# Performance work log

Hardware: AMD Instinct MI355X
Metric: run time of the kernel (lower is better)

## Reference

```python
import jax, jax.numpy as jnp
import numpy as np

PYRAMID_BINS = [512, 256, 128, 64]
ENTRY_CHANNELS = 14
CONV_FILTERS = 4
HIDDEN = 64
BATCH = 2048
LENGTH = 2048
NEG_SLOPE = 0.01  # LeakyReLU default


def setup_inputs() -> dict:
    key = jax.random.key(0)
    ks = jax.random.split(key, 9)
    nb = len(PYRAMID_BINS)
    return {
        "X": jax.random.normal(ks[0], (BATCH, ENTRY_CHANNELS, LENGTH), jnp.float32),
        "conv_w": jax.random.normal(ks[1], (nb, CONV_FILTERS, ENTRY_CHANNELS, 3), jnp.float32) * 0.1,
        "conv_b": jax.random.normal(ks[2], (nb, CONV_FILTERS), jnp.float32) * 0.1,
        "w_ih": jax.random.normal(ks[3], (nb, 4 * HIDDEN, CONV_FILTERS), jnp.float32) * 0.1,
        "w_hh": jax.random.normal(ks[4], (nb, 4 * HIDDEN, HIDDEN), jnp.float32) * 0.1,
        "b_ih": jax.random.normal(ks[5], (nb, 4 * HIDDEN), jnp.float32) * 0.1,
        "b_hh": jax.random.normal(ks[6], (nb, 4 * HIDDEN), jnp.float32) * 0.1,
        "lin_w": jax.random.normal(ks[7], (nb, 1, HIDDEN), jnp.float32) * 0.1,
        "lin_b": jax.random.normal(ks[8], (nb, 1), jnp.float32) * 0.1,
    }


def adaptive_avg_pool1d(x, out_size):
    # matches torch F.avg_pool1d with stride = L//out, kernel = L-(out-1)*stride
    L = x.shape[-1]
    stride = L // out_size
    kernel = L - (out_size - 1) * stride
    idx = jnp.arange(out_size)[:, None] * stride + jnp.arange(kernel)[None, :]  # (out, k)
    return x[..., idx].mean(axis=-1)  # (B, C, out)


def conv1d_same(x, w, b):
    # x: (B,C,L), w: (O,I,3), padding=1 -> same length
    y = jax.lax.conv_general_dilated(x, w, window_strides=(1,), padding=((1, 1),),
                                     dimension_numbers=("NCH", "OIH", "NCH"))
    return y + b[None, :, None]


def lstm_scan(xs, w_ih, w_hh, b_ih, b_hh):
    # xs: (T, B, in); PyTorch LSTMCell gate order (i, f, g, o)
    B = xs.shape[1]
    h0 = jnp.zeros((B, HIDDEN), xs.dtype)
    c0 = jnp.zeros((B, HIDDEN), xs.dtype)

    def step(carry, x):
        h, c = carry
        gates = x @ w_ih.T + b_ih + h @ w_hh.T + b_hh  # (B, 4H)
        i, f, g, o = jnp.split(gates, 4, axis=-1)
        i = jax.nn.sigmoid(i)
        f = jax.nn.sigmoid(f)
        g = jnp.tanh(g)
        o = jax.nn.sigmoid(o)
        c = f * c + i * g
        h = o * jnp.tanh(c)
        return (h, c), None

    (h, _), _ = jax.lax.scan(step, (h0, c0), xs)
    return h  # final hidden (B, H)


def reference(X, conv_w, conv_b, w_ih, w_hh, b_ih, b_hh, lin_w, lin_b):
    outs = []
    for i, bin_size in enumerate(PYRAMID_BINS):
        xp = adaptive_avg_pool1d(X, bin_size)                  # (B, C, bin)
        xc = conv1d_same(xp, conv_w[i], conv_b[i])             # (B, 4, bin)
        xc = jnp.where(xc >= 0, xc, NEG_SLOPE * xc)            # LeakyReLU
        xs = jnp.transpose(xc, (2, 0, 1))                      # (T, B, 4)
        h = lstm_scan(xs, w_ih[i], w_hh[i], b_ih[i], b_hh[i])  # (B, H)
        outs.append(h @ lin_w[i].T + lin_b[i])                 # (B, 1)
    return jnp.concatenate(outs, axis=1)                       # (B, n_bins)
```

## Files before the change

### kernel.cpp

```cpp
#include <hip/hip_runtime.h>
#include <math.h>

#define BATCH 2048
#define CIN 14
#define LEN 2048
#define NB 4
#define HID 64
#define NEG 0.01f
#define L2E 1.44269504088896f

typedef __attribute__((ext_vector_type(8))) _Float16 f16x8;
typedef __attribute__((ext_vector_type(4))) float f32x4;

__device__ __forceinline__ void conv_bin(const float* __restrict__ P, int ldp, int T,
                                         int bin,
                                         const float* __restrict__ cw,
                                         const float* __restrict__ cb,
                                         float* __restrict__ dst, int tid)
{
    const float* w = cw + (size_t)bin * 4 * CIN * 3;
    const float b0 = cb[bin * 4 + 0];
    const float b1 = cb[bin * 4 + 1];
    const float b2 = cb[bin * 4 + 2];
    const float b3 = cb[bin * 4 + 3];
    for (int t = tid; t < T; t += 256) {
        float a0 = b0, a1 = b1, a2 = b2, a3 = b3;
        for (int ci = 0; ci < CIN; ++ci) {
            float pm = (t > 0)     ? P[ci * ldp + t - 1] : 0.0f;
            float p0 =               P[ci * ldp + t];
            float pp = (t < T - 1) ? P[ci * ldp + t + 1] : 0.0f;
            const float* w0 = w + (0 * CIN + ci) * 3;
            const float* w1 = w + (1 * CIN + ci) * 3;
            const float* w2 = w + (2 * CIN + ci) * 3;
            const float* w3 = w + (3 * CIN + ci) * 3;
            a0 += w0[0] * pm + w0[1] * p0 + w0[2] * pp;
            a1 += w1[0] * pm + w1[1] * p0 + w1[2] * pp;
            a2 += w2[0] * pm + w2[1] * p0 + w2[2] * pp;
            a3 += w3[0] * pm + w3[1] * p0 + w3[2] * pp;
        }
        a0 = (a0 >= 0.0f) ? a0 : NEG * a0;
        a1 = (a1 >= 0.0f) ? a1 : NEG * a1;
        a2 = (a2 >= 0.0f) ? a2 : NEG * a2;
        a3 = (a3 >= 0.0f) ? a3 : NEG * a3;
        *reinterpret_cast<float4*>(dst + (size_t)t * 4) = make_float4(a0, a1, a2, a3);
    }
}

__global__ __launch_bounds__(256) void pool_conv_kernel(
    const float* __restrict__ X, const float* __restrict__ cw,
    const float* __restrict__ cb, float* __restrict__ xc)
{
    __shared__ float Pa[CIN][512];
    __shared__ float Pb[CIN][256];
    const int b = blockIdx.x;
    const int tid = threadIdx.x;

    for (int idx = tid; idx < CIN * 512; idx += 256) {
        int c = idx >> 9, t = idx & 511;
        const float4 v = *reinterpret_cast<const float4*>(X + ((size_t)b * CIN + c) * LEN + 4 * t);
        Pa[c][t] = 0.25f * (v.x + v.y + v.z + v.w);
    }
    __syncthreads();

    conv_bin(&Pa[0][0], 512, 512, 0, cw, cb, xc + (size_t)b * 512 * 4, tid);
    for (int idx = tid; idx < CIN * 256; idx += 256) {
        int c = idx >> 8, t = idx & 255;
        Pb[c][t] = 0.5f * (Pa[c][2 * t] + Pa[c][2 * t + 1]);
    }
    __syncthreads();

    conv_bin(&Pb[0][0], 256, 256, 1, cw, cb, xc + 4194304 + (size_t)b * 256 * 4, tid);
    for (int idx = tid; idx < CIN * 128; idx += 256) {
        int c = idx >> 7, t = idx & 127;
        Pa[c][t] = 0.5f * (Pb[c][2 * t] + Pb[c][2 * t + 1]);
    }
    __syncthreads();

    conv_bin(&Pa[0][0], 512, 128, 2, cw, cb, xc + 6291456 + (size_t)b * 128 * 4, tid);
    for (int idx = tid; idx < CIN * 64; idx += 256) {
        int c = idx >> 6, t = idx & 63;
        Pb[c][t] = 0.5f * (Pa[c][2 * t] + Pa[c][2 * t + 1]);
    }
    __syncthreads();

    conv_bin(&Pb[0][0], 256, 64, 3, cw, cb, xc + 7340032 + (size_t)b * 64 * 4, tid);
}


__global__ __launch_bounds__(256)
__attribute__((amdgpu_waves_per_eu(1, 1)))
void lstm_mfma_kernel(
    const float* __restrict__ xc,
    const float* __restrict__ wih, const float* __restrict__ whh,
    const float* __restrict__ bih, const float* __restrict__ bhh,
    const float* __restrict__ lw, const float* __restrict__ lb,
    float* __restrict__ out)
{
    __shared__ _Float16 hbuf[2][16][80];
    __shared__ _Float16 xbuf[16][65][8];
    __shared__ float    part[256];

    const int tid = threadIdx.x;
    const int w   = tid >> 6;
    const int l   = tid & 63;
    const int lm  = l & 15;
    const int lg  = l >> 4;

    const int TS[NB]     = {512, 256, 128, 64};
    const size_t OFF[NB] = {0, 4194304, 6291456, 7340032};

    const bool isBin0 = (blockIdx.x < 128);
    const int b0   = (isBin0 ? blockIdx.x : (blockIdx.x - 128)) * 16;
    const int binS = isBin0 ? 0 : 1;
    const int binE = isBin0 ? 1 : 4;

    for (int bin = binS; bin < binE; ++bin) {
        const int T = TS[bin];
        const int NW = T >> 6;
        const float* xbase = xc + OFF[bin];

        f16x8 whiF[4][2], xwB[4];
        f32x4 biasC[4];
        const int GMAP[4] = {2, 0, 1, 3};
        #pragma unroll
        for (int gs = 0; gs < 4; ++gs) {
            const int gate = GMAP[gs];
            const float sc = (gate == 2) ? (2.0f * L2E) : (-L2E);
            const int col = bin * 256 + gate * 64 + w * 16 + lm;
            const float* wr = whh + (size_t)col * 64;
            #pragma unroll
            for (int kt = 0; kt < 2; ++kt) {
                const float* p = wr + kt * 32 + lg * 8;
                const float4 u0 = *reinterpret_cast<const float4*>(p);
                const float4 u1 = *reinterpret_cast<const float4*>(p + 4);
                f16x8 h8;
                h8[0] = (_Float16)(sc * u0.x); h8[1] = (_Float16)(sc * u0.y);
                h8[2] = (_Float16)(sc * u0.z); h8[3] = (_Float16)(sc * u0.w);
                h8[4] = (_Float16)(sc * u1.x); h8[5] = (_Float16)(sc * u1.y);
                h8[6] = (_Float16)(sc * u1.z); h8[7] = (_Float16)(sc * u1.w);
                whiF[gs][kt] = h8;
            }
            const float4 wiv = *reinterpret_cast<const float4*>(wih + (size_t)col * 4);
            f16x8 xw;
            #pragma unroll
            for (int e = 0; e < 8; ++e) xw[e] = (_Float16)0.0f;
            if (lg == 0) {
                xw[0] = (_Float16)(sc * wiv.x); xw[1] = (_Float16)(sc * wiv.y);
                xw[2] = (_Float16)(sc * wiv.z); xw[3] = (_Float16)(sc * wiv.w);
            }
            xwB[gs] = xw;
            const float bv = (bih[col] + bhh[col]) * sc;
            biasC[gs] = (f32x4){bv, bv, bv, bv};
        }

        #pragma unroll
        for (int i = 0; i < 4; ++i) {
            const int idx = tid + i * 256;
            const int bb = idx >> 6, s = idx & 63;
            const float4 xv = *reinterpret_cast<const float4*>(
                xbase + ((size_t)(b0 + bb) * T + s) * 4);
            f16x8 pk;
            pk[0] = (_Float16)xv.x; pk[1] = (_Float16)xv.y;
            pk[2] = (_Float16)xv.z; pk[3] = (_Float16)xv.w;
            pk[4] = (_Float16)0.0f; pk[5] = (_Float16)0.0f;
            pk[6] = (_Float16)0.0f; pk[7] = (_Float16)0.0f;
            *reinterpret_cast<f16x8*>(&xbuf[bb][s][0]) = pk;
        }
        {
            _Float16* hz = &hbuf[0][0][0];
            #pragma unroll
            for (int i = 0; i < 5; ++i) hz[tid + i * 256] = (_Float16)0.0f;
        }
        float c4[4] = {0.0f, 0.0f, 0.0f, 0.0f};

        for (int tb = 0; tb < NW; ++tb) {
            float4 xr[4];
            #pragma unroll 2
            for (int tw = 0; tw < 64; ++tw) {
                if (tw == 32 && tb + 1 < NW) {
                    #pragma unroll
                    for (int i = 0; i < 4; ++i) {
                        const int idx = tid + i * 256;
                        const int bb = idx >> 6, s = idx & 63;
                        xr[i] = *reinterpret_cast<const float4*>(
                            xbase + ((size_t)(b0 + bb) * T + (tb + 1) * 64 + s) * 4);
                    }
                }
                __syncthreads();

                const int pp = tw & 1, pq = pp ^ 1;

                const f16x8 xfv = *reinterpret_cast<const f16x8*>(&xbuf[lm][tw][0]);
                const f16x8 zh0 = *reinterpret_cast<const f16x8*>(&hbuf[pp][lm][lg * 8]);
                const f16x8 zh1 = *reinterpret_cast<const f16x8*>(&hbuf[pp][lm][32 + lg * 8]);

                f32x4 aG = __builtin_amdgcn_mfma_f32_16x16x32_f16(xfv, xwB[0], biasC[0], 0, 0, 0);
                f32x4 aI = __builtin_amdgcn_mfma_f32_16x16x32_f16(xfv, xwB[1], biasC[1], 0, 0, 0);
                f32x4 aF = __builtin_amdgcn_mfma_f32_16x16x32_f16(xfv, xwB[2], biasC[2], 0, 0, 0);
                f32x4 aO = __builtin_amdgcn_mfma_f32_16x16x32_f16(xfv, xwB[3], biasC[3], 0, 0, 0);

                aG = __builtin_amdgcn_mfma_f32_16x16x32_f16(zh0, whiF[0][0], aG, 0, 0, 0);
                aG = __builtin_amdgcn_mfma_f32_16x16x32_f16(zh1, whiF[0][1], aG, 0, 0, 0);
                aI = __builtin_amdgcn_mfma_f32_16x16x32_f16(zh0, whiF[1][0], aI, 0, 0, 0);
                aI = __builtin_amdgcn_mfma_f32_16x16x32_f16(zh1, whiF[1][1], aI, 0, 0, 0);

                float eG[4];
                #pragma unroll
                for (int r = 0; r < 4; ++r)
                    eG[r] = __builtin_amdgcn_exp2f(fminf(aG[r], 120.0f));

                aF = __builtin_amdgcn_mfma_f32_16x16x32_f16(zh0, whiF[2][0], aF, 0, 0, 0);
                aF = __builtin_amdgcn_mfma_f32_16x16x32_f16(zh1, whiF[2][1], aF, 0, 0, 0);

                float rig[4];
                #pragma unroll
                for (int r = 0; r < 4; ++r) {
                    const float eI = __builtin_amdgcn_exp2f(aI[r]);
                    rig[r] = (eG[r] - 1.0f) *
                             __builtin_amdgcn_rcpf((1.0f + eI) * (eG[r] + 1.0f));
                }

                aO = __builtin_amdgcn_mfma_f32_16x16x32_f16(zh0, whiF[3][0], aO, 0, 0, 0);
                aO = __builtin_amdgcn_mfma_f32_16x16x32_f16(zh1, whiF[3][1], aO, 0, 0, 0);

                float C2[4];
                #pragma unroll
                for (int r = 0; r < 4; ++r) {
                    const float eF = __builtin_amdgcn_exp2f(aF[r]);
                    c4[r] = fmaf(__builtin_amdgcn_rcpf(1.0f + eF), c4[r], rig[r]);
                    C2[r] = __builtin_amdgcn_exp2f(
                        fminf((2.0f * L2E) * c4[r], 120.0f));
                }

                float oden[4];
                #pragma unroll
                for (int r = 0; r < 4; ++r)
                    oden[r] = 1.0f + __builtin_amdgcn_exp2f(aO[r]);

                const int u = w * 16 + lm;
                #pragma unroll
                for (int r = 0; r < 4; ++r) {
                    const float hv = (C2[r] - 1.0f) *
                        __builtin_amdgcn_rcpf(oden[r] * (C2[r] + 1.0f));
                    hbuf[pq][lg * 4 + r][u] = (_Float16)hv;
                }
            }
            if (tb + 1 < NW) {
                __syncthreads();
                #pragma unroll
                for (int i = 0; i < 4; ++i) {
                    const int idx = tid + i * 256;
                    const int bb = idx >> 6, s = idx & 63;
                    const float4 xv = xr[i];
                    f16x8 pk;
                    pk[0] = (_Float16)xv.x; pk[1] = (_Float16)xv.y;
                    pk[2] = (_Float16)xv.z; pk[3] = (_Float16)xv.w;
                    pk[4] = (_Float16)0.0f; pk[5] = (_Float16)0.0f;
                    pk[6] = (_Float16)0.0f; pk[7] = (_Float16)0.0f;
                    *reinterpret_cast<f16x8*>(&xbuf[bb][s][0]) = pk;
                }
            }
        }
        __syncthreads();

        {
            const int m = tid & 15, up = tid >> 4;
            const float* lwb = lw + bin * HID;
            float s = 0.0f;
            #pragma unroll
            for (int e = 0; e < 4; ++e) {
                const int uu = up * 4 + e;
                s = fmaf((float)hbuf[0][m][uu], lwb[uu], s);
            }
            part[tid] = s;
            __syncthreads();
            if (tid < 16) {
                float v = lb[bin];
                #pragma unroll
                for (int j = 0; j < 16; ++j) v += part[j * 16 + tid];
                out[(size_t)(b0 + tid) * NB + bin] = v;
            }
            __syncthreads();
        }
    }
}

extern "C" void kernel_launch(void* const* d_in, const int* in_sizes, int n_in,
                              void* d_out, int out_size, void* d_ws, size_t ws_size,
                              hipStream_t stream) {
    const float* X   = (const float*)d_in[0];
    const float* cw  = (const float*)d_in[1];
    const float* cb  = (const float*)d_in[2];
    const float* wih = (const float*)d_in[3];
    const float* whh = (const float*)d_in[4];
    const float* bih = (const float*)d_in[5];
    const float* bhh = (const float*)d_in[6];
    const float* lw  = (const float*)d_in[7];
    const float* lb  = (const float*)d_in[8];
    float* out = (float*)d_out;
    float* xc  = (float*)d_ws;

    pool_conv_kernel<<<BATCH, 256, 0, stream>>>(X, cw, cb, xc);
    lstm_mfma_kernel<<<256, 256, 0, stream>>>(xc, wih, whh, bih, bhh, lw, lb, out);
}
```

Before: 293.7 us.

## Process two batch tiles per LSTM block to interleave independent recurrences

Each LSTM block now handles two 16-sample batch groups with separate shared-memory h and x buffers, interleaving their MFMA and gate computations. The grid is halved to 128 blocks. The aim is to hide MFMA and transcendental latency in the serial recurrence through instruction-level parallelism, at the cost of using half as many CUs and more registers.

```diff
diff --git a/kernel.cpp b/kernel.cpp
--- a/kernel.cpp
+++ b/kernel.cpp
@@ -11,6 +11,8 @@
 
 typedef __attribute__((ext_vector_type(8))) _Float16 f16x8;
 typedef __attribute__((ext_vector_type(4))) float f32x4;
+
+#define MFMA16(A, B, C) __builtin_amdgcn_mfma_f32_16x16x32_f16((A), (B), (C), 0, 0, 0)
 
 __device__ __forceinline__ void conv_bin(const float* __restrict__ P, int ldp, int T,
                                          int bin,
@@ -96,8 +98,10 @@
     const float* __restrict__ lw, const float* __restrict__ lb,
     float* __restrict__ out)
 {
-    __shared__ _Float16 hbuf[2][16][80];
-    __shared__ _Float16 xbuf[16][65][8];
+    __shared__ _Float16 hbufA[2][16][80];
+    __shared__ _Float16 hbufB[2][16][80];
+    __shared__ _Float16 xbufA[16][65][8];
+    __shared__ _Float16 xbufB[16][65][8];
     __shared__ float    part[256];
 
     const int tid = threadIdx.x;
@@ -109,8 +113,10 @@
     const int TS[NB]     = {512, 256, 128, 64};
     const size_t OFF[NB] = {0, 4194304, 6291456, 7340032};
 
-    const bool isBin0 = (blockIdx.x < 128);
-    const int b0   = (isBin0 ? blockIdx.x : (blockIdx.x - 128)) * 16;
+    const bool isBin0 = (blockIdx.x < 64);
+    const int gid  = isBin0 ? blockIdx.x : (blockIdx.x - 64);
+    const int b0A  = gid * 32;
+    const int b0B  = b0A + 16;
     const int binS = isBin0 ? 0 : 1;
     const int binE = isBin0 ? 1 : 4;
 
@@ -157,24 +163,34 @@
         for (int i = 0; i < 4; ++i) {
             const int idx = tid + i * 256;
             const int bb = idx >> 6, s = idx & 63;
-            const float4 xv = *reinterpret_cast<const float4*>(
-                xbase + ((size_t)(b0 + bb) * T + s) * 4);
+            const float4 xvA = *reinterpret_cast<const float4*>(
+                xbase + ((size_t)(b0A + bb) * T + s) * 4);
+            const float4 xvB = *reinterpret_cast<const float4*>(
+                xbase + ((size_t)(b0B + bb) * T + s) * 4);
             f16x8 pk;
-            pk[0] = (_Float16)xv.x; pk[1] = (_Float16)xv.y;
-            pk[2] = (_Float16)xv.z; pk[3] = (_Float16)xv.w;
             pk[4] = (_Float16)0.0f; pk[5] = (_Float16)0.0f;
             pk[6] = (_Float16)0.0f; pk[7] = (_Float16)0.0f;
-            *reinterpret_cast<f16x8*>(&xbuf[bb][s][0]) = pk;
+            pk[0] = (_Float16)xvA.x; pk[1] = (_Float16)xvA.y;
+            pk[2] = (_Float16)xvA.z; pk[3] = (_Float16)xvA.w;
+            *reinterpret_cast<f16x8*>(&xbufA[bb][s][0]) = pk;
+            pk[0] = (_Float16)xvB.x; pk[1] = (_Float16)xvB.y;
+            pk[2] = (_Float16)xvB.z; pk[3] = (_Float16)xvB.w;
+            *reinterpret_cast<f16x8*>(&xbufB[bb][s][0]) = pk;
         }
         {
-            _Float16* hz = &hbuf[0][0][0];
-            #pragma unroll
-            for (int i = 0; i < 5; ++i) hz[tid + i * 256] = (_Float16)0.0f;
-        }
-        float c4[4] = {0.0f, 0.0f, 0.0f, 0.0f};
+            _Float16* hzA = &hbufA[0][0][0];
+            _Float16* hzB = &hbufB[0][0][0];
+            #pragma unroll
+            for (int i = 0; i < 5; ++i) {
+                hzA[tid + i * 256] = (_Float16)0.0f;
+                hzB[tid + i * 256] = (_Float16)0.0f;
+            }
+        }
+        float c4A[4] = {0.0f, 0.0f, 0.0f, 0.0f};
+        float c4B[4] = {0.0f, 0.0f, 0.0f, 0.0f};
 
         for (int tb = 0; tb < NW; ++tb) {
-            float4 xr[4];
+            float4 xrA[4], xrB[4];
             #pragma unroll 2
             for (int tw = 0; tw < 64; ++tw) {
                 if (tw == 32 && tb + 1 < NW) {
@@ -182,67 +198,110 @@
                     for (int i = 0; i < 4; ++i) {
                         const int idx = tid + i * 256;
                         const int bb = idx >> 6, s = idx & 63;
-                        xr[i] = *reinterpret_cast<const float4*>(
-                            xbase + ((size_t)(b0 + bb) * T + (tb + 1) * 64 + s) * 4);
+                        xrA[i] = *reinterpret_cast<const float4*>(
+                            xbase + ((size_t)(b0A + bb) * T + (tb + 1) * 64 + s) * 4);
+                        xrB[i] = *reinterpret_cast<const float4*>(
+                            xbase + ((size_t)(b0B + bb) * T + (tb + 1) * 64 + s) * 4);
                     }
                 }
                 __syncthreads();
 
                 const int pp = tw & 1, pq = pp ^ 1;
 
-                const f16x8 xfv = *reinterpret_cast<const f16x8*>(&xbuf[lm][tw][0]);
-                const f16x8 zh0 = *reinterpret_cast<const f16x8*>(&hbuf[pp][lm][lg * 8]);
-                const f16x8 zh1 = *reinterpret_cast<const f16x8*>(&hbuf[pp][lm][32 + lg * 8]);
-
-                f32x4 aG = __builtin_amdgcn_mfma_f32_16x16x32_f16(xfv, xwB[0], biasC[0], 0, 0, 0);
-                f32x4 aI = __builtin_amdgcn_mfma_f32_16x16x32_f16(xfv, xwB[1], biasC[1], 0, 0, 0);
-                f32x4 aF = __builtin_amdgcn_mfma_f32_16x16x32_f16(xfv, xwB[2], biasC[2], 0, 0, 0);
-                f32x4 aO = __builtin_amdgcn_mfma_f32_16x16x32_f16(xfv, xwB[3], biasC[3], 0, 0, 0);
-
-                aG = __builtin_amdgcn_mfma_f32_16x16x32_f16(zh0, whiF[0][0], aG, 0, 0, 0);
-                aG = __builtin_amdgcn_mfma_f32_16x16x32_f16(zh1, whiF[0][1], aG, 0, 0, 0);
-                aI = __builtin_amdgcn_mfma_f32_16x16x32_f16(zh0, whiF[1][0], aI, 0, 0, 0);
-                aI = __builtin_amdgcn_mfma_f32_16x16x32_f16(zh1, whiF[1][1], aI, 0, 0, 0);
-
-                float eG[4];
+                const f16x8 xfA  = *reinterpret_cast<const f16x8*>(&xbufA[lm][tw][0]);
+                const f16x8 zhA0 = *reinterpret_cast<const f16x8*>(&hbufA[pp][lm][lg * 8]);
+                const f16x8 zhA1 = *reinterpret_cast<const f16x8*>(&hbufA[pp][lm][32 + lg * 8]);
+                const f16x8 xfB  = *reinterpret_cast<const f16x8*>(&xbufB[lm][tw][0]);
+                const f16x8 zhB0 = *reinterpret_cast<const f16x8*>(&hbufB[pp][lm][lg * 8]);
+                const f16x8 zhB1 = *reinterpret_cast<const f16x8*>(&hbufB[pp][lm][32 + lg * 8]);
+
+                f32x4 aGA = MFMA16(xfA, xwB[0], biasC[0]);
+                f32x4 aIA = MFMA16(xfA, xwB[1], biasC[1]);
+                f32x4 aFA = MFMA16(xfA, xwB[2], biasC[2]);
+                f32x4 aOA = MFMA16(xfA, xwB[3], biasC[3]);
+                f32x4 aGB = MFMA16(xfB, xwB[0], biasC[0]);
+                f32x4 aIB = MFMA16(xfB, xwB[1], biasC[1]);
+                f32x4 aFB = MFMA16(xfB, xwB[2], biasC[2]);
+                f32x4 aOB = MFMA16(xfB, xwB[3], biasC[3]);
+
+                aGA = MFMA16(zhA0, whiF[0][0], aGA); aGA = MFMA16(zhA1, whiF[0][1], aGA);
+                aIA = MFMA16(zhA0, whiF[1][0], aIA); aIA = MFMA16(zhA1, whiF[1][1], aIA);
+                aGB = MFMA16(zhB0, whiF[0][0], aGB); aGB = MFMA16(zhB1, whiF[0][1], aGB);
+                aIB = MFMA16(zhB0, whiF[1][0], aIB); aIB = MFMA16(zhB1, whiF[1][1], aIB);
+
+                float eGA[4];
                 #pragma unroll
                 for (int r = 0; r < 4; ++r)
-                    eG[r] = __builtin_amdgcn_exp2f(fminf(aG[r], 120.0f));
-
-                aF = __builtin_amdgcn_mfma_f32_16x16x32_f16(zh0, whiF[2][0], aF, 0, 0, 0);
-                aF = __builtin_amdgcn_mfma_f32_16x16x32_f16(zh1, whiF[2][1], aF, 0, 0, 0);
-
-                float rig[4];
+                    eGA[r] = __builtin_amdgcn_exp2f(fminf(aGA[r], 120.0f));
+
+                aFA = MFMA16(zhA0, whiF[2][0], aFA); aFA = MFMA16(zhA1, whiF[2][1], aFA);
+                aFB = MFMA16(zhB0, whiF[2][0], aFB); aFB = MFMA16(zhB1, whiF[2][1], aFB);
+
+                float eGB[4];
+                #pragma unroll
+                for (int r = 0; r < 4; ++r)
+                    eGB[r] = __builtin_amdgcn_exp2f(fminf(aGB[r], 120.0f));
+
+                float rigA[4];
                 #pragma unroll
                 for (int r = 0; r < 4; ++r) {
-                    const float eI = __builtin_amdgcn_exp2f(aI[r]);
-                    rig[r] = (eG[r] - 1.0f) *
-                             __builtin_amdgcn_rcpf((1.0f + eI) * (eG[r] + 1.0f));
-                }
-
-                aO = __builtin_amdgcn_mfma_f32_16x16x32_f16(zh0, whiF[3][0], aO, 0, 0, 0);
-                aO = __builtin_amdgcn_mfma_f32_16x16x32_f16(zh1, whiF[3][1], aO, 0, 0, 0);
-
-                float C2[4];
+                    const float eI = __builtin_amdgcn_exp2f(aIA[r]);
+                    rigA[r] = (eGA[r] - 1.0f) *
+                              __builtin_amdgcn_rcpf((1.0f + eI) * (eGA[r] + 1.0f));
+                }
+
+                aOA = MFMA16(zhA0, whiF[3][0], aOA); aOA = MFMA16(zhA1, whiF[3][1], aOA);
+                aOB = MFMA16(zhB0, whiF[3][0], aOB); aOB = MFMA16(zhB1, whiF[3][1], aOB);
+
+                float rigB[4];
                 #pragma unroll
                 for (int r = 0; r < 4; ++r) {
-                    const float eF = __builtin_amdgcn_exp2f(aF[r]);
-                    c4[r] = fmaf(__builtin_amdgcn_rcpf(1.0f + eF), c4[r], rig[r]);
-                    C2[r] = __builtin_amdgcn_exp2f(
-                        fminf((2.0f * L2E) * c4[r], 120.0f));
-                }
-
-                float oden[4];
-                #pragma unroll
-                for (int r = 0; r < 4; ++r)
-                    oden[r] = 1.0f + __builtin_amdgcn_exp2f(aO[r]);
+                    const float eI = __builtin_amdgcn_exp2f(aIB[r]);
+                    rigB[r] = (eGB[r] - 1.0f) *
+                              __builtin_amdgcn_rcpf((1.0f + eI) * (eGB[r] + 1.0f));
+                }
 
                 const int u = w * 16 + lm;
-                #pragma unroll
-                for (int r = 0; r < 4; ++r) {
-                    const float hv = (C2[r] - 1.0f) *
-                        __builtin_amdgcn_rcpf(oden[r] * (C2[r] + 1.0f));
-                    hbuf[pq][lg * 4 + r][u] = (_Float16)hv;
+
+                {
+                    float C2[4];
+                    #pragma unroll
+                    for (int r = 0; r < 4; ++r) {
+                        const float eF = __builtin_amdgcn_exp2f(aFA[r]);
+                        c4A[r] = fmaf(__builtin_amdgcn_rcpf(1.0f + eF), c4A[r], rigA[r]);
+                        C2[r] = __builtin_amdgcn_exp2f(
+                            fminf((2.0f * L2E) * c4A[r], 120.0f));
+                    }
+                    float oden[4];
+                    #pragma unroll
+                    for (int r = 0; r < 4; ++r)
+                        oden[r] = 1.0f + __builtin_amdgcn_exp2f(aOA[r]);
+                    #pragma unroll
+                    for (int r = 0; r < 4; ++r) {
+                        const float hv = (C2[r] - 1.0f) *
+                            __builtin_amdgcn_rcpf(oden[r] * (C2[r] + 1.0f));
+                        hbufA[pq][lg * 4 + r][u] = (_Float16)hv;
+                    }
+                }
+                {
+                    float C2[4];
+                    #pragma unroll
+                    for (int r = 0; r < 4; ++r) {
+                        const float eF = __builtin_amdgcn_exp2f(aFB[r]);
+                        c4B[r] = fmaf(__builtin_amdgcn_rcpf(1.0f + eF), c4B[r], rigB[r]);
+                        C2[r] = __builtin_amdgcn_exp2f(
+                            fminf((2.0f * L2E) * c4B[r], 120.0f));
+                    }
+                    float oden[4];
+                    #pragma unroll
+                    for (int r = 0; r < 4; ++r)
+                        oden[r] = 1.0f + __builtin_amdgcn_exp2f(aOB[r]);
+                    #pragma unroll
+                    for (int r = 0; r < 4; ++r) {
+                        const float hv = (C2[r] - 1.0f) *
+                            __builtin_amdgcn_rcpf(oden[r] * (C2[r] + 1.0f));
+                        hbufB[pq][lg * 4 + r][u] = (_Float16)hv;
+                    }
                 }
             }
             if (tb + 1 < NW) {
@@ -251,13 +310,15 @@
                 for (int i = 0; i < 4; ++i) {
                     const int idx = tid + i * 256;
                     const int bb = idx >> 6, s = idx & 63;
-                    const float4 xv = xr[i];
                     f16x8 pk;
-                    pk[0] = (_Float16)xv.x; pk[1] = (_Float16)xv.y;
-                    pk[2] = (_Float16)xv.z; pk[3] = (_Float16)xv.w;
                     pk[4] = (_Float16)0.0f; pk[5] = (_Float16)0.0f;
                     pk[6] = (_Float16)0.0f; pk[7] = (_Float16)0.0f;
-                    *reinterpret_cast<f16x8*>(&xbuf[bb][s][0]) = pk;
+                    pk[0] = (_Float16)xrA[i].x; pk[1] = (_Float16)xrA[i].y;
+                    pk[2] = (_Float16)xrA[i].z; pk[3] = (_Float16)xrA[i].w;
+                    *reinterpret_cast<f16x8*>(&xbufA[bb][s][0]) = pk;
+                    pk[0] = (_Float16)xrB[i].x; pk[1] = (_Float16)xrB[i].y;
+                    pk[2] = (_Float16)xrB[i].z; pk[3] = (_Float16)xrB[i].w;
+                    *reinterpret_cast<f16x8*>(&xbufB[bb][s][0]) = pk;
                 }
             }
         }
@@ -270,7 +331,7 @@
             #pragma unroll
             for (int e = 0; e < 4; ++e) {
                 const int uu = up * 4 + e;
-                s = fmaf((float)hbuf[0][m][uu], lwb[uu], s);
+                s = fmaf((float)hbufA[0][m][uu], lwb[uu], s);
             }
             part[tid] = s;
             __syncthreads();
@@ -278,7 +339,22 @@
                 float v = lb[bin];
                 #pragma unroll
                 for (int j = 0; j < 16; ++j) v += part[j * 16 + tid];
-                out[(size_t)(b0 + tid) * NB + bin] = v;
+                out[(size_t)(b0A + tid) * NB + bin] = v;
+            }
+            __syncthreads();
+            s = 0.0f;
+            #pragma unroll
+            for (int e = 0; e < 4; ++e) {
+                const int uu = up * 4 + e;
+                s = fmaf((float)hbufB[0][m][uu], lwb[uu], s);
+            }
+            part[tid] = s;
+            __syncthreads();
+            if (tid < 16) {
+                float v = lb[bin];
+                #pragma unroll
+                for (int j = 0; j < 16; ++j) v += part[j * 16 + tid];
+                out[(size_t)(b0B + tid) * NB + bin] = v;
             }
             __syncthreads();
         }
@@ -301,5 +377,5 @@
     float* xc  = (float*)d_ws;
 
     pool_conv_kernel<<<BATCH, 256, 0, stream>>>(X, cw, cb, xc);
-    lstm_mfma_kernel<<<256, 256, 0, stream>>>(xc, wih, whh, bih, bhh, lw, lb, out);
+    lstm_mfma_kernel<<<128, 256, 0, stream>>>(xc, wih, whh, bih, bhh, lw, lb, out);
 }
```

Result: slower. 466.2 us (+58.7%).
